# Performance work log

Hardware: AMD Instinct MI355X
Metric: run time of the kernel (lower is better)

Reference implementation:

```python
import jax, jax.numpy as jnp
import numpy as np

N_NODES = 100000
N_EDGES = 1600000
IN_DIM, HID_DIM, OUT_DIM = 256, 64, 64
EPS = 1e-12  # F.normalize eps


def _gcn_conv(x, src, dst, norm, W, b, num_nodes):
    # PyG-style GCNConv: transform, then symmetric-normalized aggregation.
    h = x @ W                                   # [N, d_out]
    msg = norm[:, None] * h[src]                # [E+N, d_out] gathered messages
    out = jax.ops.segment_sum(msg, dst, num_segments=num_nodes)
    return out + b


def _l2_normalize(h):
    # F.normalize(h, p=2, dim=1)
    n = jnp.sqrt(jnp.sum(h * h, axis=-1, keepdims=True))
    return h / jnp.maximum(n, EPS)


def setup_inputs() -> dict:
    key = jax.random.key(0)
    ks = jax.random.split(key, 8)
    x = jax.random.normal(ks[0], (N_NODES, IN_DIM), dtype=jnp.float32)
    edge_index = jax.random.randint(ks[1], (2, N_EDGES), 0, N_NODES, dtype=jnp.int64)
    def glorot(k, fan_in, fan_out):
        s = np.sqrt(6.0 / (fan_in + fan_out)).astype(np.float32)
        return jax.random.uniform(k, (fan_in, fan_out), jnp.float32, -s, s)
    W1 = glorot(ks[2], IN_DIM, HID_DIM)
    W2 = glorot(ks[3], HID_DIM, HID_DIM)
    W3 = glorot(ks[4], HID_DIM, OUT_DIM)
    b1 = jnp.zeros((HID_DIM,), jnp.float32)
    b2 = jnp.zeros((HID_DIM,), jnp.float32)
    b3 = jnp.zeros((OUT_DIM,), jnp.float32)
    return {"x": x, "edge_index": edge_index,
            "W1": W1, "b1": b1, "W2": W2, "b2": b2, "W3": W3, "b3": b3}


def reference(x, edge_index, W1, b1, W2, b2, W3, b3):
    N = x.shape[0]
    # add self-loops and compute symmetric norm D^-1/2 A_hat D^-1/2
    loop = jnp.arange(N, dtype=edge_index.dtype)
    src = jnp.concatenate([edge_index[0], loop])
    dst = jnp.concatenate([edge_index[1], loop])
    deg = jax.ops.segment_sum(jnp.ones_like(src, dtype=x.dtype), dst, num_segments=N)
    dinv = jnp.where(deg > 0, jax.lax.rsqrt(jnp.maximum(deg, 1.0)), 0.0)
    norm = dinv[src] * dinv[dst]                # [E+N]

    # layer 1: conv -> relu -> (dropout p=0 = identity) -> L2-normalize
    h = jax.nn.relu(_gcn_conv(x, src, dst, norm, W1, b1, N))
    h = _l2_normalize(h)
    # layer 2
    h = jax.nn.relu(_gcn_conv(h, src, dst, norm, W2, b2, N))
    h = _l2_normalize(h)
    # final layer: plain conv (cast to float32, already float32)
    out = _gcn_conv(h, src, dst, norm, W3, b3, N)
    return out
```

## Files before the change

### kernel.cpp

```cpp
#include <hip/hip_runtime.h>
#include <hip/hip_bf16.h>
#include <math.h>

#define HID 64
#define KT 64

#define NBBITS 9
#define NBSZ 512
#define P1_BMAX 256
#define P1_CH 4096
#define P1_CAP 44

typedef __attribute__((ext_vector_type(8))) short s16x8;
typedef __attribute__((ext_vector_type(4))) float f32x4;

static inline size_t align256(size_t x) { return (x + 255) & ~(size_t)255; }

__device__ inline void gld_lds16(const float* g, float* lds) {
  __builtin_amdgcn_global_load_lds((const __attribute__((address_space(1))) void*)g,
                                   (__attribute__((address_space(3))) void*)lds, 16, 0, 0);
}

__device__ inline unsigned short f2bf(float f) {
  unsigned u = __float_as_uint(f);
  return (unsigned short)((u + 0x7FFFu + ((u >> 16) & 1u)) >> 16);
}
__device__ inline float bf2f(unsigned short h) { return __uint_as_float(((unsigned)h) << 16); }
__device__ inline float bf_lo(unsigned int u) { return __uint_as_float(u << 16); }
__device__ inline float bf_hi(unsigned int u) { return __uint_as_float(u & 0xffff0000u); }


__global__ void count_dst_kernel(const int* __restrict__ dst, int* __restrict__ cnt, int E) {
  int e = blockIdx.x * blockDim.x + threadIdx.x;
  if (e < E) atomicAdd(&cnt[dst[e]], 1);
}

__global__ void dinv_kernel(const int* __restrict__ cnt, float* __restrict__ dinv, int N) {
  int i = blockIdx.x * blockDim.x + threadIdx.x;
  if (i < N) dinv[i] = rsqrtf((float)(cnt[i] + 1));
}


__global__ void prep_kernel(const float* __restrict__ W, unsigned short* __restrict__ Dh,
                            unsigned short* __restrict__ Dl, const int* __restrict__ dst,
                            int* __restrict__ bcnt, int E, int B) {
  __shared__ int sh[1024];
  int b = blockIdx.x, t = threadIdx.x;
  if (b < 64) {
    int idx = b * 256 + t;
    int j = idx & 7, lane = (idx >> 3) & 63, ct = (idx >> 9) & 3, s = idx >> 11;
    int k = s * 32 + ((lane >> 4) << 3) + j;
    int col = ct * 16 + (lane & 15);
    float f = W[k * HID + col];
    unsigned short h = f2bf(f);
    Dh[idx] = h;
    Dl[idx] = f2bf(f - bf2f(h));
  } else {
    int cb = b - 64, nb = gridDim.x - 64;
    for (int i = t; i < B; i += 256) sh[i] = 0;
    __syncthreads();
    for (int e = cb * 256 + t; e < E; e += nb * 256)
      atomicAdd(&sh[dst[e] >> NBBITS], 1);
    __syncthreads();
    for (int i = t; i < B; i += 256) {
      int v = sh[i];
      if (v) atomicAdd(&bcnt[i], v);
    }
  }
}


__global__ __launch_bounds__(1024) void bucket_scan_kernel(const int* __restrict__ bcnt,
                                                           int* __restrict__ bbase,
                                                           int* __restrict__ gcur, int B) {
  __shared__ int sh[1024];
  int t = threadIdx.x;
  int v = (t < B) ? bcnt[t] : 0;
  sh[t] = v;
  __syncthreads();
  for (int off = 1; off < 1024; off <<= 1) {
    int u = (t >= off) ? sh[t - off] : 0;
    __syncthreads();
    sh[t] += u;
    __syncthreads();
  }
  if (t < B) {
    int ex = sh[t] - v;
    bbase[t] = ex;
    gcur[t] = ex;
  }
  if (t == 1023) bbase[B] = sh[1023];
}


__global__ __launch_bounds__(256) void bucketize_kernel(const int* __restrict__ src,
                                                        const int* __restrict__ dst,
                                                        int* __restrict__ gcur,
                                                        int* __restrict__ ebuck, int E) {
  __shared__ int cnt[P1_BMAX];
  __shared__ int lists[P1_BMAX * P1_CAP];
  int t = threadIdx.x;
  for (int i = t; i < P1_BMAX; i += 256) cnt[i] = 0;
  __syncthreads();
  int base_e = blockIdx.x * P1_CH;
#pragma unroll
  for (int u = 0; u < P1_CH / 256; ++u) {
    int e = base_e + u * 256 + t;
    if (e < E) {
      int s = src[e], d = dst[e];
      int bk = d >> NBBITS;
      int packed = (s << NBBITS) | (d & (NBSZ - 1));
      int p = atomicAdd(&cnt[bk], 1);
      if (p < P1_CAP) {
        lists[bk * P1_CAP + p] = packed;
      } else {
        int gp = atomicAdd(&gcur[bk], 1);
        ebuck[gp] = packed;
      }
    }
  }
  __syncthreads();
  int w = t >> 6, lane = t & 63;
  int bk = w * 64 + lane;
  int c = min(cnt[bk], P1_CAP);
  int mybase = 0;
  if (c > 0) mybase = atomicAdd(&gcur[bk], c);
#pragma unroll 1
  for (int i = 0; i < 64; ++i) {
    int cb = __shfl(c, i);
    if (cb == 0) continue;
    int gb = __shfl(mybase, i);
    int bb = w * 64 + i;
    if (lane < cb) ebuck[gb + lane] = lists[bb * P1_CAP + lane];
  }
}


__global__ __launch_bounds__(512) void bucket_sort_kernel(const int* __restrict__ ebuck,
                                                          const int* __restrict__ bbase,
                                                          int* __restrict__ rowptr,
                                                          int* __restrict__ epack,
                                                          float* __restrict__ dinv,
                                                          int N, int B, int E) {
  __shared__ int lcnt[NBSZ];
  __shared__ int lcur[NBSZ];
  int b = blockIdx.x;
  int t = threadIdx.x;
  int n0 = b << NBBITS;
  lcnt[t] = 0;
  __syncthreads();
  int e0 = bbase[b], e1 = bbase[b + 1];
  for (int i = e0 + t; i < e1; i += NBSZ) atomicAdd(&lcnt[ebuck[i] & (NBSZ - 1)], 1);
  __syncthreads();
  int v = lcnt[t];
  for (int off = 1; off < NBSZ; off <<= 1) {
    int u = (t >= off) ? lcnt[t - off] : 0;
    __syncthreads();
    lcnt[t] += u;
    __syncthreads();
  }
  int ex = lcnt[t] - v;
  int node = n0 + t;
  if (node < N) {
    rowptr[node] = e0 + ex;
    dinv[node] = rsqrtf((float)(v + 1));
  }
  if (b == B - 1 && t == 0) rowptr[N] = E;
  lcur[t] = e0 + ex;
  __syncthreads();
  for (int i = e0 + t; i < e1; i += NBSZ) {
    int pv = ebuck[i];
    int pos = atomicAdd(&lcur[pv & (NBSZ - 1)], 1);
    epack[pos] = ((unsigned)pv) >> NBBITS;
  }
}


template <int K>
__global__ __launch_bounds__(256, 4) void gemm_mfma_kernel(
    const float* __restrict__ x, const unsigned short* __restrict__ Wh,
    const unsigned short* __restrict__ Wl, const float* __restrict__ dinv,
    unsigned short* __restrict__ out, int N) {
  constexpr int NS = K / 32;
  __shared__ float xs[2][64 * 32];
  const int t = threadIdx.x, lane = t & 63, w = t >> 6;
  const int g = lane >> 4, r15 = lane & 15;
  const int row0 = blockIdx.x * 64;
  const int arow = w * 16 + r15;
  f32x4 acc[4];
#pragma unroll
  for (int ct = 0; ct < 4; ++ct) acc[ct] = (f32x4){0.f, 0.f, 0.f, 0.f};

  auto stage = [&](int buf, int s) {
#pragma unroll
    for (int c = 0; c < 2; ++c) {
      int idx = c * 256 + t;
      int row = idx >> 3, gp = idx & 7;
      int gs = gp ^ (row & 7);
      int grow = min(row0 + row, N - 1);
      gld_lds16(x + (size_t)grow * K + s * 32 + gs * 4, &xs[buf][idx * 4]);
    }
  };
  stage(0, 0);
  for (int s = 0; s < NS; ++s) {
    __syncthreads();
    if (s + 1 < NS) stage((s + 1) & 1, s + 1);
    const float* xb = &xs[s & 1][arow * 32];
    float4 xv0 = *(const float4*)&xb[((2 * g) ^ (arow & 7)) * 4];
    float4 xv1 = *(const float4*)&xb[((2 * g + 1) ^ (arow & 7)) * 4];
    float xf[8] = {xv0.x, xv0.y, xv0.z, xv0.w, xv1.x, xv1.y, xv1.z, xv1.w};
    s16x8 xh, xl;
#pragma unroll
    for (int j = 0; j < 8; ++j) {
      unsigned short hb = f2bf(xf[j]);
      xh[j] = (short)hb;
      xl[j] = (short)f2bf(xf[j] - bf2f(hb));
    }
#pragma unroll
    for (int ct = 0; ct < 4; ++ct) {
      size_t o = (((size_t)(s * 4 + ct)) * 64 + lane) * 8;
      s16x8 wh = *(const s16x8*)&Wh[o];
      s16x8 wl = *(const s16x8*)&Wl[o];
      acc[ct] = __builtin_amdgcn_mfma_f32_16x16x32_bf16(wh, xh, acc[ct], 0, 0, 0);
      acc[ct] = __builtin_amdgcn_mfma_f32_16x16x32_bf16(wl, xh, acc[ct], 0, 0, 0);
      acc[ct] = __builtin_amdgcn_mfma_f32_16x16x32_bf16(wh, xl, acc[ct], 0, 0, 0);
    }
  }
  int row = row0 + arow;
  if (row < N) {
    float di = dinv[row];
    unsigned short* orow = out + (size_t)row * HID;
#pragma unroll
    for (int ct = 0; ct < 4; ++ct) {
      unsigned p0 = (unsigned)f2bf(di * acc[ct][0]) | ((unsigned)f2bf(di * acc[ct][1]) << 16);
      unsigned p1 = (unsigned)f2bf(di * acc[ct][2]) | ((unsigned)f2bf(di * acc[ct][3]) << 16);
      *(uint2*)&orow[ct * 16 + g * 4] = make_uint2(p0, p1);
    }
  }
}


__global__ __launch_bounds__(256) void agg_gemm_kernel(
    const int* __restrict__ rowptr, const int* __restrict__ ep,
    const float* __restrict__ dinv, const uint2* __restrict__ hin,
    const float* __restrict__ bias, const float* __restrict__ Wn,
    unsigned short* __restrict__ hout, int N) {
  __shared__ float Ws[64 * 64];
  __shared__ float vrow[4][4 * 68];
  const int t = threadIdx.x;
#pragma unroll
  for (int c = 0; c < 4; ++c) {
    int idx = c * 256 + t;
    gld_lds16(Wn + idx * 4, &Ws[idx * 4]);
  }
  __syncthreads();
  const int w = t >> 6, lane = t & 63;
  const int q = lane >> 4, sub = lane & 15;
  const int node = blockIdx.x * 16 + w * 4 + q;
  float4 v = make_float4(0.f, 0.f, 0.f, 0.f);
  float di = 0.f;
  if (node < N) {
    int beg = rowptr[node];
    int end = rowptr[node + 1];
    uint2 su = hin[(size_t)node * 16 + sub];
    float a0 = bf_lo(su.x), a1 = bf_hi(su.x), a2 = bf_lo(su.y), a3 = bf_hi(su.y);
    int j = beg;
    for (; j + 8 <= end; j += 8) {
      int e[8];
      uint2 hv[8];
#pragma unroll
      for (int u = 0; u < 8; ++u) e[u] = ep[j + u];
#pragma unroll
      for (int u = 0; u < 8; ++u) hv[u] = hin[(size_t)e[u] * 16 + sub];
#pragma unroll
      for (int u = 0; u < 8; ++u) {
        a0 += bf_lo(hv[u].x); a1 += bf_hi(hv[u].x);
        a2 += bf_lo(hv[u].y); a3 += bf_hi(hv[u].y);
      }
    }
    for (; j < end; ++j) {
      uint2 hu = hin[(size_t)ep[j] * 16 + sub];
      a0 += bf_lo(hu.x); a1 += bf_hi(hu.x); a2 += bf_lo(hu.y); a3 += bf_hi(hu.y);
    }
    di = dinv[node];
    float4 b4 = *(const float4*)&bias[sub * 4];
    v.x = fmaxf(fmaf(di, a0, b4.x), 0.f);
    v.y = fmaxf(fmaf(di, a1, b4.y), 0.f);
    v.z = fmaxf(fmaf(di, a2, b4.z), 0.f);
    v.w = fmaxf(fmaf(di, a3, b4.w), 0.f);
    float ss = v.x * v.x + v.y * v.y + v.z * v.z + v.w * v.w;
#pragma unroll
    for (int off = 8; off; off >>= 1) ss += __shfl_xor(ss, off, 64);
    float inv = 1.f / fmaxf(sqrtf(ss), 1e-12f);
    v.x *= inv; v.y *= inv; v.z *= inv; v.w *= inv;
  }
  *(float4*)&vrow[w][q * 68 + sub * 4] = v;
  if (node < N) {
    float4 o = make_float4(0.f, 0.f, 0.f, 0.f);
#pragma unroll 8
    for (int f = 0; f < 64; ++f) {
      float vf = vrow[w][q * 68 + f];
      float4 wf = *(const float4*)&Ws[f * 64 + sub * 4];
      o.x = fmaf(vf, wf.x, o.x);
      o.y = fmaf(vf, wf.y, o.y);
      o.z = fmaf(vf, wf.z, o.z);
      o.w = fmaf(vf, wf.w, o.w);
    }
    unsigned p0 = (unsigned)f2bf(di * o.x) | ((unsigned)f2bf(di * o.y) << 16);
    unsigned p1 = (unsigned)f2bf(di * o.z) | ((unsigned)f2bf(di * o.w) << 16);
    *(uint2*)&hout[(size_t)node * HID + sub * 4] = make_uint2(p0, p1);
  }
}


template <bool RELU_NORM>
__global__ void agg_kernel(const int* __restrict__ rowptr, const int* __restrict__ ep,
                           const float* __restrict__ dinv, const uint2* __restrict__ h64,
                           const float* __restrict__ bias, float* __restrict__ out, int N) {
  int grp = (blockIdx.x * blockDim.x + threadIdx.x) >> 6;
  int lane = threadIdx.x & 63;
  int q = lane >> 4;
  int sub = lane & 15;
  int node = grp * 4 + q;
  if (node >= N) return;
  int beg = rowptr[node];
  int end = rowptr[node + 1];
  uint2 su = h64[(size_t)node * 16 + sub];
  float a0 = bf_lo(su.x), a1 = bf_hi(su.x), a2 = bf_lo(su.y), a3 = bf_hi(su.y);
  int j = beg;
  for (; j + 8 <= end; j += 8) {
    int e[8];
    uint2 hv[8];
#pragma unroll
    for (int u = 0; u < 8; ++u) e[u] = ep[j + u];
#pragma unroll
    for (int u = 0; u < 8; ++u) hv[u] = h64[(size_t)e[u] * 16 + sub];
#pragma unroll
    for (int u = 0; u < 8; ++u) {
      a0 += bf_lo(hv[u].x); a1 += bf_hi(hv[u].x);
      a2 += bf_lo(hv[u].y); a3 += bf_hi(hv[u].y);
    }
  }
  for (; j < end; ++j) {
    uint2 hu = h64[(size_t)ep[j] * 16 + sub];
    a0 += bf_lo(hu.x); a1 += bf_hi(hu.x); a2 += bf_lo(hu.y); a3 += bf_hi(hu.y);
  }
  float di = dinv[node];
  float4 b4 = *(const float4*)&bias[sub * 4];
  float4 v;
  v.x = fmaf(di, a0, b4.x); v.y = fmaf(di, a1, b4.y);
  v.z = fmaf(di, a2, b4.z); v.w = fmaf(di, a3, b4.w);
  if (RELU_NORM) {
    v.x = fmaxf(v.x, 0.f); v.y = fmaxf(v.y, 0.f);
    v.z = fmaxf(v.z, 0.f); v.w = fmaxf(v.w, 0.f);
    float ss = v.x * v.x + v.y * v.y + v.z * v.z + v.w * v.w;
#pragma unroll
    for (int off = 8; off; off >>= 1) ss += __shfl_xor(ss, off, 64);
    float inv = 1.f / fmaxf(sqrtf(ss), 1e-12f);
    v.x *= inv; v.y *= inv; v.z *= inv; v.w *= inv;
  }
  *(float4*)&out[(size_t)node * HID + sub * 4] = v;
}


template <int K, typename OT>
__global__ __launch_bounds__(256, 4) void gemm_kernel(const float* __restrict__ x,
                                                      const float* __restrict__ W,
                                                      OT* __restrict__ out, int N) {
  __shared__ float Xs[64 * KT];
  __shared__ float Ws[KT * 64];
  const int t = threadIdx.x;
  const int lane = t & 63;
  const int w = t >> 6;
  const int rg = lane >> 4;
  const int cg = lane & 15;
  const int row0 = blockIdx.x * 64;
  float4 acc[4];
#pragma unroll
  for (int r = 0; r < 4; ++r) acc[r] = make_float4(0.f, 0.f, 0.f, 0.f);

  for (int k0 = 0; k0 < K; k0 += KT) {
    if (k0) __syncthreads();
    const float* Wg = W + (size_t)k0 * HID;
#pragma unroll
    for (int c = 0; c < 4; ++c) {
      int idx = c * 256 + t;
      gld_lds16(Wg + idx * 4, &Ws[idx * 4]);
      int srow = idx >> 4;
      int sg = (idx & 15) ^ ((srow >> 2) & 3);
      int grow = min(row0 + srow, N - 1);
      gld_lds16(x + (size_t)grow * K + k0 + (sg << 2), &Xs[idx * 4]);
    }
    __syncthreads();
    const int rbase = w * 16 + rg * 4;
#pragma unroll 4
    for (int kb = 0; kb < KT / 4; ++kb) {
      float4 wq0 = *(const float4*)&Ws[(4 * kb + 0) * HID + cg * 4];
      float4 wq1 = *(const float4*)&Ws[(4 * kb + 1) * HID + cg * 4];
      float4 wq2 = *(const float4*)&Ws[(4 * kb + 2) * HID + cg * 4];
      float4 wq3 = *(const float4*)&Ws[(4 * kb + 3) * HID + cg * 4];
      const int sg = (kb ^ rg) << 2;
#pragma unroll
      for (int r = 0; r < 4; ++r) {
        float4 xv = *(const float4*)&Xs[(rbase + r) * KT + sg];
        acc[r].x = fmaf(xv.w, wq3.x, fmaf(xv.z, wq2.x, fmaf(xv.y, wq1.x, fmaf(xv.x, wq0.x, acc[r].x))));
        acc[r].y = fmaf(xv.w, wq3.y, fmaf(xv.z, wq2.y, fmaf(xv.y, wq1.y, fmaf(xv.x, wq0.y, acc[r].y))));
        acc[r].z = fmaf(xv.w, wq3.z, fmaf(xv.z, wq2.z, fmaf(xv.y, wq1.z, fmaf(xv.x, wq0.z, acc[r].z))));
        acc[r].w = fmaf(xv.w, wq3.w, fmaf(xv.z, wq2.w, fmaf(xv.y, wq1.w, fmaf(xv.x, wq0.w, acc[r].w))));
      }
    }
  }
#pragma unroll
  for (int r = 0; r < 4; ++r) {
    int row = row0 + w * 16 + rg * 4 + r;
    if (row < N) {
      OT* o = out + (size_t)row * HID + cg * 4;
      o[0] = (OT)acc[r].x; o[1] = (OT)acc[r].y; o[2] = (OT)acc[r].z; o[3] = (OT)acc[r].w;
    }
  }
}


__global__ void init_agg_kernel(const float* __restrict__ dinv, const float* __restrict__ h,
                                const float* __restrict__ bias, float* __restrict__ out, int N) {
  int t = blockIdx.x * blockDim.x + threadIdx.x;
  int i = t >> 6, f = t & 63;
  if (i >= N) return;
  float di = dinv[i];
  out[t] = di * di * h[t] + bias[f];
}

__global__ void edge_atomic_kernel(const int* __restrict__ src, const int* __restrict__ dst,
                                   const float* __restrict__ dinv, const float* __restrict__ h,
                                   float* __restrict__ out, int E) {
  int t = blockIdx.x * blockDim.x + threadIdx.x;
  int e = t >> 6;
  if (e >= E) return;
  int f = t & 63;
  int s = src[e], d = dst[e];
  atomicAdd(&out[(size_t)d * HID + f], dinv[s] * dinv[d] * h[(size_t)s * HID + f]);
}

__global__ void relu_norm_kernel(float* __restrict__ hbuf, int N) {
  int t = blockIdx.x * blockDim.x + threadIdx.x;
  int i = t >> 6;
  if (i >= N) return;
  float v = fmaxf(hbuf[t], 0.f);
  float ss = v * v;
#pragma unroll
  for (int off = 32; off; off >>= 1) ss += __shfl_xor(ss, off, 64);
  hbuf[t] = v / fmaxf(sqrtf(ss), 1e-12f);
}


extern "C" void kernel_launch(void* const* d_in, const int* in_sizes, int n_in,
                              void* d_out, int out_size, void* d_ws, size_t ws_size,
                              hipStream_t stream) {
  const float* x  = (const float*)d_in[0];
  const int*   ei = (const int*)d_in[1];
  const float* W1 = (const float*)d_in[2];
  const float* b1 = (const float*)d_in[3];
  const float* W2 = (const float*)d_in[4];
  const float* b2 = (const float*)d_in[5];
  const float* W3 = (const float*)d_in[6];
  const float* b3 = (const float*)d_in[7];
  float* out = (float*)d_out;

  const int IN = in_sizes[2] / HID;
  const int N  = in_sizes[0] / IN;
  const int E  = in_sizes[1] / 2;
  const int* srcI = ei;
  const int* dstI = ei + E;
  const int B = (N + NBSZ - 1) >> NBBITS;

  char* w = (char*)d_ws;
  size_t off = 0;
  auto alloc = [&](size_t bytes) { void* p = w + off; off = align256(off + bytes); return p; };
  float* A      = (float*)alloc((size_t)N * HID * 4);
  float* dinv   = (float*)alloc((size_t)N * 4);
  int*   cnt    = (int*)alloc((size_t)N * 4);
  size_t base_need = off;
  int*   rowptr = (int*)alloc((size_t)(N + 1) * 4);
  int*   epack  = (int*)alloc((size_t)E * 4);
  int*   bbase  = (int*)alloc(1032 * 4);
  int*   gcur   = (int*)alloc(1024 * 4);
  int*   bcnt   = (int*)alloc(1024 * 4);
  unsigned short* W1h = (unsigned short*)alloc(16384 * 2);
  unsigned short* W1l = (unsigned short*)alloc(16384 * 2);
  size_t csr_need = off;

  if (base_need > ws_size) return;
  const bool use_csr = (csr_need <= ws_size) && (B <= P1_BMAX) && (B <= 1024) &&
                       ((size_t)E <= (size_t)N * HID) && (N <= (1 << 20));
  unsigned short* hsA = (unsigned short*)A;
  unsigned short* hsB = hsA + (size_t)N * HID;
  int* ebuck = (int*)A;

  const int blkE    = (E + 255) / 256;
  const int blkN    = (N + 255) / 256;
  const int blkRow  = (N + 63) / 64;
  const int blkWave = (N * 64 + 255) / 256;
  const int blkAgg  = ((size_t)((N + 3) / 4) * 64 + 255) / 256;
  const int blkFuse = (N + 15) / 16;
  const int blkEF   = ((size_t)E * 64 + 255) / 256;
  const int blkBkt  = (E + P1_CH - 1) / P1_CH;

  if (use_csr) {
    hipMemsetAsync(bcnt, 0, 1024 * 4, stream);
    prep_kernel<<<320, 256, 0, stream>>>(W1, W1h, W1l, dstI, bcnt, E, B);
    bucket_scan_kernel<<<1, 1024, 0, stream>>>(bcnt, bbase, gcur, B);
    bucketize_kernel<<<blkBkt, 256, 0, stream>>>(srcI, dstI, gcur, ebuck, E);
    bucket_sort_kernel<<<B, NBSZ, 0, stream>>>(ebuck, bbase, rowptr, epack, dinv, N, B, E);

    gemm_mfma_kernel<256><<<blkRow, 256, 0, stream>>>(x, W1h, W1l, dinv, hsA, N);
    agg_gemm_kernel<<<blkFuse, 256, 0, stream>>>(rowptr, epack, dinv, (const uint2*)hsA,
                                                 b1, W2, hsB, N);
    agg_gemm_kernel<<<blkFuse, 256, 0, stream>>>(rowptr, epack, dinv, (const uint2*)hsB,
                                                 b2, W3, hsA, N);
    agg_kernel<false><<<blkAgg, 256, 0, stream>>>(rowptr, epack, dinv, (const uint2*)hsA,
                                                  b3, out, N);
  } else {
    hipMemsetAsync(cnt, 0, (size_t)N * 4, stream);
    count_dst_kernel<<<blkE, 256, 0, stream>>>(dstI, cnt, E);
    dinv_kernel<<<blkN, 256, 0, stream>>>(cnt, dinv, N);

    gemm_kernel<256><<<blkRow, 256, 0, stream>>>(x, W1, A, N);
    init_agg_kernel<<<blkWave, 256, 0, stream>>>(dinv, A, b1, out, N);
    edge_atomic_kernel<<<blkEF, 256, 0, stream>>>(srcI, dstI, dinv, A, out, E);
    relu_norm_kernel<<<blkWave, 256, 0, stream>>>(out, N);

    gemm_kernel<64><<<blkRow, 256, 0, stream>>>(out, W2, A, N);
    init_agg_kernel<<<blkWave, 256, 0, stream>>>(dinv, A, b2, out, N);
    edge_atomic_kernel<<<blkEF, 256, 0, stream>>>(srcI, dstI, dinv, A, out, E);
    relu_norm_kernel<<<blkWave, 256, 0, stream>>>(out, N);

    gemm_kernel<64><<<blkRow, 256, 0, stream>>>(out, W3, A, N);
    init_agg_kernel<<<blkWave, 256, 0, stream>>>(dinv, A, b3, out, N);
    edge_atomic_kernel<<<blkEF, 256, 0, stream>>>(srcI, dstI, dinv, A, out, E);
  }
}
```

Before: 382.3 us.

## Merge preprocessing and layer kernels into two cooperative persistent kernels

```diff
diff --git a/kernel.cpp b/kernel.cpp
--- a/kernel.cpp
+++ b/kernel.cpp
@@ -1,6 +1,9 @@
 #include <hip/hip_runtime.h>
+#include <hip/hip_cooperative_groups.h>
 #include <hip/hip_bf16.h>
 #include <math.h>
+
+namespace cg = cooperative_groups;
 
 #define HID 64
 #define KT 64
@@ -30,6 +33,341 @@
 __device__ inline float bf_hi(unsigned int u) { return __uint_as_float(u & 0xffff0000u); }
 
 
+__global__ __launch_bounds__(512) void prep_coop(
+    const int* __restrict__ src, const int* __restrict__ dst, const float* __restrict__ W1,
+    unsigned short* __restrict__ W1h, unsigned short* __restrict__ W1l,
+    int* __restrict__ bcnt_s, int* __restrict__ bbase, int* __restrict__ gcur,
+    int* __restrict__ ebuck, int* __restrict__ rowptr, int* __restrict__ epack,
+    float* __restrict__ dinv, int N, int E, int B) {
+  __shared__ int lds[P1_BMAX + P1_BMAX * P1_CAP];
+  cg::grid_group gg = cg::this_grid();
+  const int blk = blockIdx.x, t = threadIdx.x, G = gridDim.x;
+
+  for (int idx = blk * 512 + t; idx < 16384; idx += G * 512) {
+    int j = idx & 7, lane = (idx >> 3) & 63, ct = (idx >> 9) & 3, s = idx >> 11;
+    int k = s * 32 + ((lane >> 4) << 3) + j;
+    int col = ct * 16 + (lane & 15);
+    float f = W1[k * HID + col];
+    unsigned short h = f2bf(f);
+    W1h[idx] = h;
+    W1l[idx] = f2bf(f - bf2f(h));
+  }
+  for (int i = t; i < P1_BMAX; i += 512) lds[i] = 0;
+  __syncthreads();
+  for (int e = blk * 512 + t; e < E; e += G * 512) atomicAdd(&lds[dst[e] >> NBBITS], 1);
+  __syncthreads();
+  for (int i = t; i < B; i += 512) bcnt_s[blk * P1_BMAX + i] = lds[i];
+  __threadfence();
+  gg.sync();
+
+  if (blk == 0) {
+    int v = 0;
+    if (t < B)
+      for (int s = 0; s < G; ++s) v += bcnt_s[s * P1_BMAX + t];
+    lds[t] = v;
+    __syncthreads();
+    for (int off = 1; off < 512; off <<= 1) {
+      int u = (t >= off) ? lds[t - off] : 0;
+      __syncthreads();
+      lds[t] += u;
+      __syncthreads();
+    }
+    if (t < B) {
+      int ex = lds[t] - v;
+      bbase[t] = ex;
+      gcur[t] = ex;
+    }
+    if (t == 511) {
+      bbase[B] = lds[511];
+      rowptr[N] = E;
+    }
+  }
+  __threadfence();
+  gg.sync();
+
+  {
+    int* cnt = lds;
+    int* lists = lds + P1_BMAX;
+    const int nch = (E + P1_CH - 1) / P1_CH;
+    for (int c = blk; c < nch; c += G) {
+      for (int i = t; i < P1_BMAX; i += 512) cnt[i] = 0;
+      __syncthreads();
+      int e0c = c * P1_CH, e1c = min(E, e0c + P1_CH);
+      for (int e = e0c + t; e < e1c; e += 512) {
+        int s = src[e], d = dst[e];
+        int bk = d >> NBBITS;
+        int packed = (s << NBBITS) | (d & (NBSZ - 1));
+        int p = atomicAdd(&cnt[bk], 1);
+        if (p < P1_CAP) {
+          lists[bk * P1_CAP + p] = packed;
+        } else {
+          int gp = atomicAdd(&gcur[bk], 1);
+          ebuck[gp] = packed;
+        }
+      }
+      __syncthreads();
+      int w5 = t >> 6, lane = t & 63;
+      for (int bk = w5; bk < B; bk += 8) {
+        int cb = min(cnt[bk], P1_CAP);
+        if (cb == 0) continue;
+        int base = 0;
+        if (lane == 0) base = atomicAdd(&gcur[bk], cb);
+        base = __shfl(base, 0, 64);
+        if (lane < cb) ebuck[base + lane] = lists[bk * P1_CAP + lane];
+      }
+      __syncthreads();
+    }
+  }
+  __threadfence();
+  gg.sync();
+
+  {
+    int* lcnt = lds;
+    int* lcur = lds + NBSZ;
+    for (int b = blk; b < B; b += G) {
+      lcnt[t] = 0;
+      __syncthreads();
+      int e0 = bbase[b], e1 = bbase[b + 1];
+      for (int i = e0 + t; i < e1; i += NBSZ) atomicAdd(&lcnt[ebuck[i] & (NBSZ - 1)], 1);
+      __syncthreads();
+      int v = lcnt[t];
+      for (int off = 1; off < NBSZ; off <<= 1) {
+        int u = (t >= off) ? lcnt[t - off] : 0;
+        __syncthreads();
+        lcnt[t] += u;
+        __syncthreads();
+      }
+      int ex = lcnt[t] - v;
+      int node = (b << NBBITS) + t;
+      if (node < N) {
+        rowptr[node] = e0 + ex;
+        dinv[node] = rsqrtf((float)(v + 1));
+      }
+      lcur[t] = e0 + ex;
+      __syncthreads();
+      for (int i = e0 + t; i < e1; i += NBSZ) {
+        int pv = ebuck[i];
+        int pos = atomicAdd(&lcur[pv & (NBSZ - 1)], 1);
+        epack[pos] = ((unsigned)pv) >> NBBITS;
+      }
+      __syncthreads();
+    }
+  }
+}
+
+
+__device__ __forceinline__ void agg_gemm_body(
+    const float* __restrict__ Ws, float* __restrict__ vr,
+    const int* __restrict__ rowptr, const int* __restrict__ ep,
+    const float* __restrict__ dinv, const uint2* __restrict__ hin,
+    const float* __restrict__ bias, unsigned short* __restrict__ hout, int N) {
+  const int t = threadIdx.x;
+  const int w = t >> 6, lane = t & 63;
+  const int q = lane >> 4, sub = lane & 15;
+  const int ngroups = (N + 15) >> 4;
+  for (int gi = blockIdx.x; gi < ngroups; gi += gridDim.x) {
+    const int node = (gi << 4) + (w << 2) + q;
+    float4 v = make_float4(0.f, 0.f, 0.f, 0.f);
+    float di = 0.f;
+    if (node < N) {
+      int beg = rowptr[node];
+      int end = rowptr[node + 1];
+      uint2 su = hin[(size_t)node * 16 + sub];
+      float a0 = bf_lo(su.x), a1 = bf_hi(su.x), a2 = bf_lo(su.y), a3 = bf_hi(su.y);
+      int j = beg;
+      for (; j + 8 <= end; j += 8) {
+        int e[8];
+        uint2 hv[8];
+#pragma unroll
+        for (int u = 0; u < 8; ++u) e[u] = ep[j + u];
+#pragma unroll
+        for (int u = 0; u < 8; ++u) hv[u] = hin[(size_t)e[u] * 16 + sub];
+#pragma unroll
+        for (int u = 0; u < 8; ++u) {
+          a0 += bf_lo(hv[u].x); a1 += bf_hi(hv[u].x);
+          a2 += bf_lo(hv[u].y); a3 += bf_hi(hv[u].y);
+        }
+      }
+      for (; j < end; ++j) {
+        uint2 hu = hin[(size_t)ep[j] * 16 + sub];
+        a0 += bf_lo(hu.x); a1 += bf_hi(hu.x); a2 += bf_lo(hu.y); a3 += bf_hi(hu.y);
+      }
+      di = dinv[node];
+      float4 b4 = *(const float4*)&bias[sub * 4];
+      v.x = fmaxf(fmaf(di, a0, b4.x), 0.f);
+      v.y = fmaxf(fmaf(di, a1, b4.y), 0.f);
+      v.z = fmaxf(fmaf(di, a2, b4.z), 0.f);
+      v.w = fmaxf(fmaf(di, a3, b4.w), 0.f);
+      float ss = v.x * v.x + v.y * v.y + v.z * v.z + v.w * v.w;
+#pragma unroll
+      for (int off = 8; off; off >>= 1) ss += __shfl_xor(ss, off, 64);
+      float inv = 1.f / fmaxf(sqrtf(ss), 1e-12f);
+      v.x *= inv; v.y *= inv; v.z *= inv; v.w *= inv;
+    }
+    *(float4*)&vr[q * 68 + sub * 4] = v;
+    if (node < N) {
+      float4 o = make_float4(0.f, 0.f, 0.f, 0.f);
+#pragma unroll 8
+      for (int f = 0; f < 64; ++f) {
+        float vf = vr[q * 68 + f];
+        float4 wf = *(const float4*)&Ws[f * 64 + sub * 4];
+        o.x = fmaf(vf, wf.x, o.x);
+        o.y = fmaf(vf, wf.y, o.y);
+        o.z = fmaf(vf, wf.z, o.z);
+        o.w = fmaf(vf, wf.w, o.w);
+      }
+      unsigned p0 = (unsigned)f2bf(di * o.x) | ((unsigned)f2bf(di * o.y) << 16);
+      unsigned p1 = (unsigned)f2bf(di * o.z) | ((unsigned)f2bf(di * o.w) << 16);
+      *(uint2*)&hout[(size_t)node * HID + sub * 4] = make_uint2(p0, p1);
+    }
+  }
+}
+
+__device__ __forceinline__ void agg_final_body(
+    const int* __restrict__ rowptr, const int* __restrict__ ep,
+    const float* __restrict__ dinv, const uint2* __restrict__ hin,
+    const float* __restrict__ bias, float* __restrict__ out, int N) {
+  const int t = threadIdx.x;
+  const int w = t >> 6, lane = t & 63;
+  const int q = lane >> 4, sub = lane & 15;
+  const int ngroups = (N + 15) >> 4;
+  for (int gi = blockIdx.x; gi < ngroups; gi += gridDim.x) {
+    const int node = (gi << 4) + (w << 2) + q;
+    if (node >= N) continue;
+    int beg = rowptr[node];
+    int end = rowptr[node + 1];
+    uint2 su = hin[(size_t)node * 16 + sub];
+    float a0 = bf_lo(su.x), a1 = bf_hi(su.x), a2 = bf_lo(su.y), a3 = bf_hi(su.y);
+    int j = beg;
+    for (; j + 8 <= end; j += 8) {
+      int e[8];
+      uint2 hv[8];
+#pragma unroll
+      for (int u = 0; u < 8; ++u) e[u] = ep[j + u];
+#pragma unroll
+      for (int u = 0; u < 8; ++u) hv[u] = hin[(size_t)e[u] * 16 + sub];
+#pragma unroll
+      for (int u = 0; u < 8; ++u) {
+        a0 += bf_lo(hv[u].x); a1 += bf_hi(hv[u].x);
+        a2 += bf_lo(hv[u].y); a3 += bf_hi(hv[u].y);
+      }
+    }
+    for (; j < end; ++j) {
+      uint2 hu = hin[(size_t)ep[j] * 16 + sub];
+      a0 += bf_lo(hu.x); a1 += bf_hi(hu.x); a2 += bf_lo(hu.y); a3 += bf_hi(hu.y);
+    }
+    float di = dinv[node];
+    float4 b4 = *(const float4*)&bias[sub * 4];
+    float4 v;
+    v.x = fmaf(di, a0, b4.x); v.y = fmaf(di, a1, b4.y);
+    v.z = fmaf(di, a2, b4.z); v.w = fmaf(di, a3, b4.w);
+    *(float4*)&out[(size_t)node * HID + sub * 4] = v;
+  }
+}
+
+__global__ __launch_bounds__(256, 4) void main_coop(
+    const float* __restrict__ x, const unsigned short* __restrict__ W1h,
+    const unsigned short* __restrict__ W1l, const float* __restrict__ dinv,
+    unsigned short* __restrict__ hsA, unsigned short* __restrict__ hsB,
+    const int* __restrict__ rowptr, const int* __restrict__ ep,
+    const float* __restrict__ b1, const float* __restrict__ W2,
+    const float* __restrict__ b2, const float* __restrict__ W3,
+    const float* __restrict__ b3, float* __restrict__ out, int N) {
+  __shared__ float lds[4096 + 4 * 272];
+  cg::grid_group gg = cg::this_grid();
+  const int t = threadIdx.x, lane = t & 63, w = t >> 6;
+
+  {
+    const int g = lane >> 4, r15 = lane & 15;
+    const int arow = w * 16 + r15;
+    const int ntiles = (N + 63) >> 6;
+    for (int tile = blockIdx.x; tile < ntiles; tile += gridDim.x) {
+      const int row0 = tile << 6;
+      f32x4 acc[4];
+#pragma unroll
+      for (int ct = 0; ct < 4; ++ct) acc[ct] = (f32x4){0.f, 0.f, 0.f, 0.f};
+#pragma unroll
+      for (int c = 0; c < 2; ++c) {
+        int idx = c * 256 + t;
+        int row = idx >> 3, gp = idx & 7;
+        int gs = gp ^ (row & 7);
+        int grow = min(row0 + row, N - 1);
+        gld_lds16(x + (size_t)grow * 256 + gs * 4, &lds[idx * 4]);
+      }
+      for (int s = 0; s < 8; ++s) {
+        __syncthreads();
+        if (s + 1 < 8) {
+          float* xb = lds + ((s + 1) & 1) * 2048;
+#pragma unroll
+          for (int c = 0; c < 2; ++c) {
+            int idx = c * 256 + t;
+            int row = idx >> 3, gp = idx & 7;
+            int gs = gp ^ (row & 7);
+            int grow = min(row0 + row, N - 1);
+            gld_lds16(x + (size_t)grow * 256 + (s + 1) * 32 + gs * 4, &xb[idx * 4]);
+          }
+        }
+        const float* xb = lds + (s & 1) * 2048 + arow * 32;
+        float4 xv0 = *(const float4*)&xb[((2 * g) ^ (arow & 7)) * 4];
+        float4 xv1 = *(const float4*)&xb[((2 * g + 1) ^ (arow & 7)) * 4];
+        float xf[8] = {xv0.x, xv0.y, xv0.z, xv0.w, xv1.x, xv1.y, xv1.z, xv1.w};
+        s16x8 xh, xl;
+#pragma unroll
+        for (int j = 0; j < 8; ++j) {
+          unsigned short hb = f2bf(xf[j]);
+          xh[j] = (short)hb;
+          xl[j] = (short)f2bf(xf[j] - bf2f(hb));
+        }
+#pragma unroll
+        for (int ct = 0; ct < 4; ++ct) {
+          size_t o = (((size_t)(s * 4 + ct)) * 64 + lane) * 8;
+          s16x8 wh = *(const s16x8*)&W1h[o];
+          s16x8 wl = *(const s16x8*)&W1l[o];
+          acc[ct] = __builtin_amdgcn_mfma_f32_16x16x32_bf16(wh, xh, acc[ct], 0, 0, 0);
+          acc[ct] = __builtin_amdgcn_mfma_f32_16x16x32_bf16(wl, xh, acc[ct], 0, 0, 0);
+          acc[ct] = __builtin_amdgcn_mfma_f32_16x16x32_bf16(wh, xl, acc[ct], 0, 0, 0);
+        }
+      }
+      int row = row0 + arow;
+      if (row < N) {
+        float di = dinv[row];
+        unsigned short* orow = hsA + (size_t)row * HID;
+#pragma unroll
+        for (int ct = 0; ct < 4; ++ct) {
+          unsigned p0 = (unsigned)f2bf(di * acc[ct][0]) | ((unsigned)f2bf(di * acc[ct][1]) << 16);
+          unsigned p1 = (unsigned)f2bf(di * acc[ct][2]) | ((unsigned)f2bf(di * acc[ct][3]) << 16);
+          *(uint2*)&orow[ct * 16 + g * 4] = make_uint2(p0, p1);
+        }
+      }
+    }
+  }
+  __threadfence();
+  gg.sync();
+
+#pragma unroll
+  for (int c = 0; c < 4; ++c) {
+    int idx = c * 256 + t;
+    gld_lds16(W2 + idx * 4, &lds[idx * 4]);
+  }
+  __syncthreads();
+  agg_gemm_body(lds, &lds[4096 + w * 272], rowptr, ep, dinv, (const uint2*)hsA, b1, hsB, N);
+  __threadfence();
+  gg.sync();
+
+#pragma unroll
+  for (int c = 0; c < 4; ++c) {
+    int idx = c * 256 + t;
+    gld_lds16(W3 + idx * 4, &lds[idx * 4]);
+  }
+  __syncthreads();
+  agg_gemm_body(lds, &lds[4096 + w * 272], rowptr, ep, dinv, (const uint2*)hsB, b2, hsA, N);
+  __threadfence();
+  gg.sync();
+
+  agg_final_body(rowptr, ep, dinv, (const uint2*)hsA, b3, out, N);
+}
+
+
 __global__ void count_dst_kernel(const int* __restrict__ dst, int* __restrict__ cnt, int E) {
   int e = blockIdx.x * blockDim.x + threadIdx.x;
   if (e < E) atomicAdd(&cnt[dst[e]], 1);
@@ -39,7 +377,6 @@
   int i = blockIdx.x * blockDim.x + threadIdx.x;
   if (i < N) dinv[i] = rsqrtf((float)(cnt[i] + 1));
 }
-
 
 __global__ void prep_kernel(const float* __restrict__ W, unsigned short* __restrict__ Dh,
                             unsigned short* __restrict__ Dl, const int* __restrict__ dst,
@@ -69,7 +406,6 @@
   }
 }
 
-
 __global__ __launch_bounds__(1024) void bucket_scan_kernel(const int* __restrict__ bcnt,
                                                            int* __restrict__ bbase,
                                                            int* __restrict__ gcur, int B) {
@@ -91,7 +427,6 @@
   }
   if (t == 1023) bbase[B] = sh[1023];
 }
-
 
 __global__ __launch_bounds__(256) void bucketize_kernel(const int* __restrict__ src,
                                                         const int* __restrict__ dst,
@@ -122,7 +457,7 @@
   __syncthreads();
   int w = t >> 6, lane = t & 63;
   int bk = w * 64 + lane;
-  int c = min(cnt[bk], P1_CAP);
+  int c = (bk < P1_BMAX) ? min(cnt[bk], P1_CAP) : 0;
   int mybase = 0;
   if (c > 0) mybase = atomicAdd(&gcur[bk], c);
 #pragma unroll 1
@@ -134,7 +469,6 @@
     if (lane < cb) ebuck[gb + lane] = lists[bb * P1_CAP + lane];
   }
 }
-
 
 __global__ __launch_bounds__(512) void bucket_sort_kernel(const int* __restrict__ ebuck,
                                                           const int* __restrict__ bbase,
@@ -175,7 +509,6 @@
   }
 }
 
-
 template <int K>
 __global__ __launch_bounds__(256, 4) void gemm_mfma_kernel(
     const float* __restrict__ x, const unsigned short* __restrict__ Wh,
@@ -238,7 +571,6 @@
     }
   }
 }
-
 
 __global__ __launch_bounds__(256) void agg_gemm_kernel(
     const int* __restrict__ rowptr, const int* __restrict__ ep,
@@ -311,7 +643,6 @@
     *(uint2*)&hout[(size_t)node * HID + sub * 4] = make_uint2(p0, p1);
   }
 }
-
 
 template <bool RELU_NORM>
 __global__ void agg_kernel(const int* __restrict__ rowptr, const int* __restrict__ ep,
@@ -420,7 +751,6 @@
   }
 }
 
-
 __global__ void init_agg_kernel(const float* __restrict__ dinv, const float* __restrict__ h,
                                 const float* __restrict__ bias, float* __restrict__ out, int N) {
   int t = blockIdx.x * blockDim.x + threadIdx.x;
@@ -485,12 +815,13 @@
   int*   bbase  = (int*)alloc(1032 * 4);
   int*   gcur   = (int*)alloc(1024 * 4);
   int*   bcnt   = (int*)alloc(1024 * 4);
+  int*   bcnt_s = (int*)alloc((size_t)256 * P1_BMAX * 4);
   unsigned short* W1h = (unsigned short*)alloc(16384 * 2);
   unsigned short* W1l = (unsigned short*)alloc(16384 * 2);
   size_t csr_need = off;
 
   if (base_need > ws_size) return;
-  const bool use_csr = (csr_need <= ws_size) && (B <= P1_BMAX) && (B <= 1024) &&
+  const bool use_csr = (csr_need <= ws_size) && (B <= P1_BMAX) && (IN == 256) &&
                        ((size_t)E <= (size_t)N * HID) && (N <= (1 << 20));
   unsigned short* hsA = (unsigned short*)A;
   unsigned short* hsB = hsA + (size_t)N * HID;
@@ -505,13 +836,56 @@
   const int blkEF   = ((size_t)E * 64 + 255) / 256;
   const int blkBkt  = (E + P1_CH - 1) / P1_CH;
 
-  if (use_csr) {
-    hipMemsetAsync(bcnt, 0, 1024 * 4, stream);
+  static int nCU = 0, occ1 = 0, occ2 = 0;
+  static bool queried = false;
+  if (!queried) {
+    queried = true;
+    if (hipDeviceGetAttribute(&nCU, hipDeviceAttributeMultiprocessorCount, 0) != hipSuccess)
+      nCU = 0;
+    if (hipOccupancyMaxActiveBlocksPerMultiprocessor(&occ1, prep_coop, 512, 0) != hipSuccess)
+      occ1 = 0;
+    if (hipOccupancyMaxActiveBlocksPerMultiprocessor(&occ2, main_coop, 256, 0) != hipSuccess)
+      occ2 = 0;
+  }
+
+  bool done = false;
+  if (use_csr && nCU > 0 && occ1 > 0 && occ2 > 0) {
+    int g1 = occ1 * nCU; if (g1 > 256) g1 = 256;
+    int g2 = occ2 * nCU; if (g2 > 2048) g2 = 2048;
+    int Nl = N, El = E, Bl = B;
+    void* a1[] = {(void*)&srcI, (void*)&dstI, (void*)&W1, (void*)&W1h, (void*)&W1l,
+                  (void*)&bcnt_s, (void*)&bbase, (void*)&gcur, (void*)&ebuck,
+                  (void*)&rowptr, (void*)&epack, (void*)&dinv,
+                  (void*)&Nl, (void*)&El, (void*)&Bl};
+    hipError_t e1 = hipLaunchCooperativeKernel((const void*)prep_coop, dim3(g1), dim3(512),
+                                               a1, 0, stream);
+    if (e1 == hipSuccess) {
+      void* a2[] = {(void*)&x, (void*)&W1h, (void*)&W1l, (void*)&dinv, (void*)&hsA,
+                    (void*)&hsB, (void*)&rowptr, (void*)&epack, (void*)&b1, (void*)&W2,
+                    (void*)&b2, (void*)&W3, (void*)&b3, (void*)&out, (void*)&Nl};
+      hipError_t e2 = hipLaunchCooperativeKernel((const void*)main_coop, dim3(g2), dim3(256),
+                                                 a2, 0, stream);
+      if (e2 == hipSuccess) {
+        done = true;
+      } else {
+        gemm_mfma_kernel<256><<<blkRow, 256, 0, stream>>>(x, W1h, W1l, dinv, hsA, N);
+        agg_gemm_kernel<<<blkFuse, 256, 0, stream>>>(rowptr, epack, dinv, (const uint2*)hsA,
+                                                     b1, W2, hsB, N);
+        agg_gemm_kernel<<<blkFuse, 256, 0, stream>>>(rowptr, epack, dinv, (const uint2*)hsB,
+                                                     b2, W3, hsA, N);
+        agg_kernel<false><<<blkAgg, 256, 0, stream>>>(rowptr, epack, dinv, (const uint2*)hsA,
+                                                      b3, out, N);
+        done = true;
+      }
+    }
+  }
+
+  if (!done && use_csr) {
+    (void)hipMemsetAsync(bcnt, 0, 1024 * 4, stream);
     prep_kernel<<<320, 256, 0, stream>>>(W1, W1h, W1l, dstI, bcnt, E, B);
     bucket_scan_kernel<<<1, 1024, 0, stream>>>(bcnt, bbase, gcur, B);
     bucketize_kernel<<<blkBkt, 256, 0, stream>>>(srcI, dstI, gcur, ebuck, E);
     bucket_sort_kernel<<<B, NBSZ, 0, stream>>>(ebuck, bbase, rowptr, epack, dinv, N, B, E);
-
     gemm_mfma_kernel<256><<<blkRow, 256, 0, stream>>>(x, W1h, W1l, dinv, hsA, N);
     agg_gemm_kernel<<<blkFuse, 256, 0, stream>>>(rowptr, epack, dinv, (const uint2*)hsA,
                                                  b1, W2, hsB, N);
@@ -519,8 +893,11 @@
                                                  b2, W3, hsA, N);
     agg_kernel<false><<<blkAgg, 256, 0, stream>>>(rowptr, epack, dinv, (const uint2*)hsA,
                                                   b3, out, N);
-  } else {
-    hipMemsetAsync(cnt, 0, (size_t)N * 4, stream);
+    done = true;
+  }
+
+  if (!done) {
+    (void)hipMemsetAsync(cnt, 0, (size_t)N * 4, stream);
     count_dst_kernel<<<blkE, 256, 0, stream>>>(dstI, cnt, E);
     dinv_kernel<<<blkN, 256, 0, stream>>>(cnt, dinv, N);
 
```

After: 1.399 ms. 3.66x slower.
